# Optimization experiments

Hardware: AMD Instinct MI355X
Metric: run time of the kernel (lower is better)

## Reference

```python
import jax, jax.numpy as jnp
import numpy as np

K_SIZE = 5
SIGMA_IMG = 0.2
SIGMA_VGG = 0.02
BN_EPS = 1e-5
NORM = 2.0  # 2 * len(GPU_IDS), assuming 1 device


def _window_shifts(x, k):
    # x: (n, C, H, W) -> (n, C, H, W, k*k) neighbor values for every offset in
    # the k x k window, zero-padded at image borders.
    r = k // 2
    n, C, H, W = x.shape
    xp = jnp.pad(x, ((0, 0), (0, 0), (r, r), (r, r)))
    cols = [xp[:, :, di:di + H, dj:dj + W] for di in range(k) for dj in range(k)]
    return jnp.stack(cols, axis=-1)


def _modularity(img, seg, k, sigma):
    # img: (n, C, H, W) feature map; seg: (n, K, H, W) soft assignments.
    n, K, H, W = seg.shape
    seg2 = _window_shifts(seg, k)                                  # (n,K,H,W,kk)
    img2 = _window_shifts(img, k)                                  # (n,C,H,W,kk)
    valid = _window_shifts(jnp.ones((1, 1, H, W), img.dtype), k)[:, 0]  # (1,H,W,kk)
    d2 = ((img[..., None] - img2) ** 2).sum(axis=1)                # (n,H,W,kk)
    w12 = jax.lax.stop_gradient(jnp.exp(-d2 / (2.0 * sigma * sigma)) * valid)
    # numerator: sum over pixels & pairs of p1*p2*w12, per (n, K)
    num = jnp.einsum('nkhw,nkhwp,nhwp->nk', seg, seg2, w12)
    # p1 (sum over pairs of p1/n_pairs) == seg; w1 = sum over pairs of w12
    w1 = w12.sum(axis=-1)                                          # (n,H,W)
    den = jnp.einsum('nhw,nkhw->nk', w1, seg)
    rel = num / den                                                # (n,K)
    return rel.sum(axis=1) / (K * n)                               # (n,)


def _conv(x, w, b):
    y = jax.lax.conv_general_dilated(x, w, (1, 1), 'SAME',
                                     dimension_numbers=('NCHW', 'OIHW', 'NCHW'))
    return y + b[None, :, None, None]


def _maxpool2(x):
    return jax.lax.reduce_window(x, -jnp.inf, jax.lax.max,
                                 (1, 1, 2, 2), (1, 1, 2, 2), 'VALID')


def _avgpool2(x):
    n, c, h, w = x.shape
    return x.reshape(n, c, h // 2, 2, w // 2, 2).mean(axis=(3, 5))


def _vgg8(x, w1, b1, w2, b2, w3, b3, w4, b4):
    # VGG16 features[:8]: conv1_1, conv1_2, maxpool, conv2_1, conv2_2 (relu each)
    x = jax.nn.relu(_conv(x, w1, b1))
    x = jax.nn.relu(_conv(x, w2, b2))
    x = _maxpool2(x)
    x = jax.nn.relu(_conv(x, w3, b3))
    x = jax.nn.relu(_conv(x, w4, b4))
    return x


def _batchnorm(x):
    # fresh BatchNorm2d in training mode (weight=1, bias=0), then detach
    m = x.mean(axis=(0, 2, 3), keepdims=True)
    v = x.var(axis=(0, 2, 3), keepdims=True)
    return jax.lax.stop_gradient((x - m) / jnp.sqrt(v + BN_EPS))


def setup_inputs() -> dict:
    key = jax.random.key(0)
    ks = jax.random.split(key, 6)
    images = jax.random.uniform(ks[0], (4, 3, 128, 128), jnp.float32)
    seg = jax.random.uniform(ks[1], (4, 8, 128, 128), jnp.float32)
    segmentation = seg / seg.sum(axis=1, keepdims=True)
    w1 = jax.random.normal(ks[2], (64, 3, 3, 3), jnp.float32) * 0.1
    w2 = jax.random.normal(ks[3], (64, 64, 3, 3), jnp.float32) * 0.05
    w3 = jax.random.normal(ks[4], (128, 64, 3, 3), jnp.float32) * 0.05
    w4 = jax.random.normal(ks[5], (128, 128, 3, 3), jnp.float32) * 0.03
    return {'images': images, 'segmentation': segmentation,
            'w1': w1, 'b1': jnp.zeros(64), 'w2': w2, 'b2': jnp.zeros(64),
            'w3': w3, 'b3': jnp.zeros(128), 'w4': w4, 'b4': jnp.zeros(128)}


def reference(images, segmentation, w1, b1, w2, b2, w3, b3, w4, b4):
    fich = _batchnorm(_vgg8(images, w1, b1, w2, b2, w3, b3, w4, b4))  # (n,128,64,64)
    images_n = _batchnorm(images)
    down_seg = segmentation
    while down_seg.shape[-1] != fich.shape[-1]:
        down_seg = _avgpool2(down_seg)
    loss = (_modularity(fich, down_seg, K_SIZE, SIGMA_VGG).sum()
            + _modularity(images_n, segmentation, K_SIZE, SIGMA_IMG).sum())
    return loss / NORM
```

## Files before the change

### kernel.cpp

```cpp
#include <hip/hip_runtime.h>
#include <hip/hip_bf16.h>
#include <math.h>

typedef __attribute__((ext_vector_type(8))) short short8;
typedef __attribute__((ext_vector_type(4))) float floatx4;
typedef unsigned short ushortT;

__device__ inline short f2bf(float v) {
    __hip_bfloat16 h = __float2bfloat16(v);
    union { __hip_bfloat16 h; short s; } u; u.h = h; return u.s;
}

#define OFF_C2    0
#define OFF_PAD4  8388608
#define OFF_FICH  12849152
#define OFF_PAD2  21237760
#define OFF_PAD3  29890560
#define OFF_WP2   32120832
#define OFF_WP3   32194560
#define OFF_WP4   32342016
#define OFF_ST    33947648
#define OFF_P64   33951744
#define OFF_P128  33968128
#define OFF_PBN   34033664
#define OFF_PIMG  34295808

__global__ __launch_bounds__(256) void prologue(
    char* ws, const float* __restrict__ images,
    const float* __restrict__ w1, const float* __restrict__ b1,
    const float* __restrict__ w2, const float* __restrict__ w3,
    const float* __restrict__ w4)
{
    __shared__ float plds[3 * 720];
    __shared__ float rs[256], rs2[256];

    int b = blockIdx.x;
    int tid = threadIdx.x;

    if (b >= 1362) {
        int bid = b - 1362;
        int txt = bid & 7; bid >>= 3;
        int tyt = bid & 7; bid >>= 3;
        int ocg = bid & 7; bid >>= 3;
        int n = bid;
        int x0 = txt * 16, y0 = tyt * 16;
        int tx = tid & 15, ty = tid >> 4;
        short* outp = (short*)(ws + OFF_PAD2);

        for (int i = tid; i < 972; i += 256) {
            int cc = i / 324; int rem = i - cc * 324;
            int r = rem / 18, c = rem - r * 18;
            int y = y0 - 1 + r, x = x0 - 1 + c;
            float v = 0.f;
            if ((unsigned)y < 128u && (unsigned)x < 128u)
                v = images[((size_t)(n * 3 + cc) * 128 + y) * 128 + x];
            plds[cc * 720 + r * 40 + c] = v;
        }
        __syncthreads();

        float acc[8];
#pragma unroll
        for (int oc = 0; oc < 8; ++oc) acc[oc] = 0.f;
        const float* w_g = w1 + (size_t)(ocg * 8) * 27;
#pragma unroll
        for (int cc = 0; cc < 3; ++cc) {
            const float* base = &plds[cc * 720 + ty * 40 + tx];
            float i00 = base[0],  i01 = base[1],  i02 = base[2];
            float i10 = base[40], i11 = base[41], i12 = base[42];
            float i20 = base[80], i21 = base[81], i22 = base[82];
            const float* wp = w_g + cc * 9;
#pragma unroll
            for (int oc = 0; oc < 8; ++oc) {
                const float* wq = wp + oc * 27;
                float a = acc[oc];
                a = fmaf(wq[0], i00, a); a = fmaf(wq[1], i01, a); a = fmaf(wq[2], i02, a);
                a = fmaf(wq[3], i10, a); a = fmaf(wq[4], i11, a); a = fmaf(wq[5], i12, a);
                a = fmaf(wq[6], i20, a); a = fmaf(wq[7], i21, a); a = fmaf(wq[8], i22, a);
                acc[oc] = a;
            }
        }
        int oy = y0 + ty, ox = x0 + tx;
        short* o = outp + ((size_t)(n * 130 + oy + 1) * 130 + ox + 1) * 64 + ocg * 8;
#pragma unroll
        for (int oc = 0; oc < 8; ++oc) {
            float v = fmaxf(acc[oc] + b1[ocg * 8 + oc], 0.f);
            o[oc] = f2bf(v);
        }
        return;
    }

    if (b < 162) {
        int t = b * 256 + tid;
        short* base; int Hp, Wp, C; int idx;
        if (t < 16512)      { base = (short*)(ws + OFF_PAD2); Hp = 130; Wp = 130; C = 64;  idx = t; }
        else if (t < 24832) { base = (short*)(ws + OFF_PAD3); Hp = 66;  Wp = 66;  C = 64;  idx = t - 16512; }
        else if (t < 41472) { base = (short*)(ws + OFF_PAD4); Hp = 66;  Wp = 66;  C = 128; idx = t - 24832; }
        else return;
        int c8 = idx % (C / 8); int rest = idx / (C / 8);
        int haloPx = 2 * Wp + 2 * (Hp - 2);
        int p = rest % haloPx; int n = rest / haloPx;
        int y, x;
        if (p < Wp)          { y = 0;      x = p; }
        else if (p < 2 * Wp) { y = Hp - 1; x = p - Wp; }
        else { int j = p - 2 * Wp; y = 1 + (j >> 1); x = (j & 1) ? (Wp - 1) : 0; }
        short8 z = {0, 0, 0, 0, 0, 0, 0, 0};
        *(short8*)&base[((size_t)((n * Hp + y) * Wp) + x) * C + c8 * 8] = z;
        return;
    }
    if (b < 1170) {
        int e = (b - 162) * 256 + tid;
        const float* w; short* wp; int CIN, NTALL;
        if (e < 36864)       { w = w2; wp = (short*)(ws + OFF_WP2); CIN = 64;  NTALL = 4; }
        else if (e < 110592) { e -= 36864;  w = w3; wp = (short*)(ws + OFF_WP3); CIN = 64;  NTALL = 8; }
        else if (e < 258048) { e -= 110592; w = w4; wp = (short*)(ws + OFF_WP4); CIN = 128; NTALL = 8; }
        else return;
        int j = e & 7; int L = (e >> 3) & 63; int rest = e >> 9;
        int nt = rest % NTALL; int rest2 = rest / NTALL;
        int KT = CIN / 32;
        int kt = rest2 % KT; int t = rest2 / KT;
        int oc = nt * 16 + (L & 15);
        int ci = kt * 32 + (L >> 4) * 8 + j;
        wp[e] = f2bf(w[((size_t)oc * CIN + ci) * 9 + t]);
        return;
    }
    {
        float* part = (float*)(ws + OFF_PIMG);
        int bb = b - 1170;
        int c = bb >> 6, chunk = bb & 63;
        int base = chunk * 1024 + tid;
        float s = 0.f, s2 = 0.f;
#pragma unroll
        for (int k = 0; k < 4; ++k) {
            int i = base + k * 256;
            int n = i >> 14, hw = i & 16383;
            float v = images[(((size_t)(n * 3 + c)) << 14) + hw];
            s += v; s2 = fmaf(v, v, s2);
        }
        rs[tid] = s; rs2[tid] = s2;
        __syncthreads();
        for (int k = 128; k > 0; k >>= 1) {
            if (tid < k) { rs[tid] += rs[tid + k]; rs2[tid] += rs2[tid + k]; }
            __syncthreads();
        }
        if (tid == 0) { part[bb * 2] = rs[0]; part[bb * 2 + 1] = rs2[0]; }
    }
}

__global__ __launch_bounds__(256) void conv2_pool(
    const short* __restrict__ inp,
    const short* __restrict__ wp,
    const float* __restrict__ bias,
    short* __restrict__ outp)
{
    constexpr int CIN = 64;
    constexpr int Hp = 130, Wp = 130;

    int bid = blockIdx.x;
    int xtb = bid & 1; bid >>= 1;
    int yp = bid & 63; bid >>= 6;
    int n = bid;
    int y0 = yp * 2;
    int x0 = xtb * 64;

    int tid = threadIdx.x;
    int wv = tid >> 6, lane = tid & 63;
    int lm = lane & 15, q = lane >> 4;
    int px0 = x0 + 16 * wv;

    floatx4 acc0[4], acc1[4];
#pragma unroll
    for (int t = 0; t < 4; ++t) {
        acc0[t] = (floatx4){0.f, 0.f, 0.f, 0.f};
        acc1[t] = (floatx4){0.f, 0.f, 0.f, 0.f};
    }

    const short* a_m = inp + lm * CIN + q * 8;
    const short* wbase = wp + (size_t)lane * 8;

    for (int kt = 0; kt < 2; ++kt) {
        int kofs = kt * 32;
#pragma unroll
        for (int s = 0; s < 3; ++s) {
            const short* acol = a_m + ((size_t)((n * Hp + y0) * Wp) + px0 + s) * CIN + kofs;
            short8 av0 = *(const short8*)(acol);
            short8 av1 = *(const short8*)(acol + (size_t)Wp * CIN);
            short8 av2 = *(const short8*)(acol + (size_t)2 * Wp * CIN);
            short8 av3 = *(const short8*)(acol + (size_t)3 * Wp * CIN);
#pragma unroll
            for (int r = 0; r < 3; ++r) {
                const short* bp = wbase + (size_t)(((r * 3 + s) * 2 + kt) * 4) * 512;
                short8 b0 = *(const short8*)bp;
                short8 b1 = *(const short8*)(bp + 512);
                short8 b2 = *(const short8*)(bp + 1024);
                short8 b3 = *(const short8*)(bp + 1536);
                short8 ar  = (r == 0) ? av0 : ((r == 1) ? av1 : av2);
                short8 ar1 = (r == 0) ? av1 : ((r == 1) ? av2 : av3);
                acc0[0] = __builtin_amdgcn_mfma_f32_16x16x32_bf16(ar, b0, acc0[0], 0, 0, 0);
                acc0[1] = __builtin_amdgcn_mfma_f32_16x16x32_bf16(ar, b1, acc0[1], 0, 0, 0);
                acc0[2] = __builtin_amdgcn_mfma_f32_16x16x32_bf16(ar, b2, acc0[2], 0, 0, 0);
                acc0[3] = __builtin_amdgcn_mfma_f32_16x16x32_bf16(ar, b3, acc0[3], 0, 0, 0);
                acc1[0] = __builtin_amdgcn_mfma_f32_16x16x32_bf16(ar1, b0, acc1[0], 0, 0, 0);
                acc1[1] = __builtin_amdgcn_mfma_f32_16x16x32_bf16(ar1, b1, acc1[1], 0, 0, 0);
                acc1[2] = __builtin_amdgcn_mfma_f32_16x16x32_bf16(ar1, b2, acc1[2], 0, 0, 0);
                acc1[3] = __builtin_amdgcn_mfma_f32_16x16x32_bf16(ar1, b3, acc1[3], 0, 0, 0);
            }
        }
    }

    int ox = (px0 + q * 4) >> 1;
#pragma unroll
    for (int t = 0; t < 4; ++t) {
        int oc = t * 16 + lm;
        float bs = bias[oc];
        float v00 = fmaxf(acc0[t][0] + bs, 0.f);
        float v01 = fmaxf(acc0[t][1] + bs, 0.f);
        float v02 = fmaxf(acc0[t][2] + bs, 0.f);
        float v03 = fmaxf(acc0[t][3] + bs, 0.f);
        float v10 = fmaxf(acc1[t][0] + bs, 0.f);
        float v11 = fmaxf(acc1[t][1] + bs, 0.f);
        float v12 = fmaxf(acc1[t][2] + bs, 0.f);
        float v13 = fmaxf(acc1[t][3] + bs, 0.f);
        float m0 = fmaxf(fmaxf(v00, v01), fmaxf(v10, v11));
        float m1 = fmaxf(fmaxf(v02, v03), fmaxf(v12, v13));
        short* o = outp + ((size_t)(n * 66 + yp + 1) * 66 + ox + 1) * 64 + oc;
        o[0]  = f2bf(m0);
        o[64] = f2bf(m1);
    }
}

template<int CIN, int COUT, int H, int W, int OUTMODE>
__global__ __launch_bounds__(256) void conv_mfma2(
    const short* __restrict__ inp, const short* __restrict__ wp,
    const float* __restrict__ bias, void* __restrict__ outv)
{
    constexpr int KT = CIN / 32;
    constexpr int NTALL = COUT / 16;
    constexpr int NTB = COUT / 64;
    constexpr int TPR = W / 64;
    constexpr int Hp = H + 2, Wp = W + 2;

    int bm = blockIdx.x / NTB;
    int bn = blockIdx.x - bm * NTB;
    int n = bm / (H * TPR);
    int rem = bm - n * (H * TPR);
    int y = rem / TPR;
    int x0 = (rem - y * TPR) * 64;

    int tid = threadIdx.x;
    int wv = tid >> 6, lane = tid & 63;
    int lm = lane & 15, q = lane >> 4;
    int px0 = x0 + 16 * wv;
    int ntb = bn * 4;

    floatx4 acc[4];
#pragma unroll
    for (int t = 0; t < 4; ++t) acc[t] = (floatx4){0.f, 0.f, 0.f, 0.f};

    const short* a_m = inp + lm * CIN + q * 8;
    const short* wbase = wp + ((size_t)ntb * 64 + lane) * 8;

    for (int kt = 0; kt < KT; ++kt) {
        int kofs = kt * 32;
#pragma unroll
        for (int r = 0; r < 3; ++r) {
            const short* arow = a_m + (size_t)((n * Hp + y + r) * Wp + px0) * CIN + kofs;
#pragma unroll
            for (int s = 0; s < 3; ++s) {
                short8 av = *(const short8*)(arow + s * CIN);
                const short* bp = wbase + (size_t)(((r * 3 + s) * KT + kt) * NTALL) * 512;
                short8 b0 = *(const short8*)bp;
                short8 b1 = *(const short8*)(bp + 512);
                short8 b2 = *(const short8*)(bp + 1024);
                short8 b3 = *(const short8*)(bp + 1536);
                acc[0] = __builtin_amdgcn_mfma_f32_16x16x32_bf16(av, b0, acc[0], 0, 0, 0);
                acc[1] = __builtin_amdgcn_mfma_f32_16x16x32_bf16(av, b1, acc[1], 0, 0, 0);
                acc[2] = __builtin_amdgcn_mfma_f32_16x16x32_bf16(av, b2, acc[2], 0, 0, 0);
                acc[3] = __builtin_amdgcn_mfma_f32_16x16x32_bf16(av, b3, acc[3], 0, 0, 0);
            }
        }
    }

#pragma unroll
    for (int t = 0; t < 4; ++t) {
        int oc = (ntb + t) * 16 + lm;
        float bs = bias[oc];
#pragma unroll
        for (int i = 0; i < 4; ++i) {
            int px = px0 + q * 4 + i;
            float v = fmaxf(acc[t][i] + bs, 0.f);
            if constexpr (OUTMODE == 0) {
                ((short*)outv)[((size_t)(n * H + y) * W + px) * COUT + oc] = f2bf(v);
            } else if constexpr (OUTMODE == 1) {
                ((short*)outv)[((size_t)(n * Hp + y + 1) * Wp + px + 1) * COUT + oc] = f2bf(v);
            } else {
                ((float*)outv)[((size_t)(n * H + y) * W + px) * COUT + oc] = v;
            }
        }
    }
}

__global__ __launch_bounds__(256) void conv4_bn(
    const short* __restrict__ inp,
    const short* __restrict__ wp,
    const float* __restrict__ bias,
    float* __restrict__ out,
    float* __restrict__ part)
{
    constexpr int CIN = 128;
    constexpr int Hp = 66, Wp = 66;

    int bm = blockIdx.x >> 1;
    int bn = blockIdx.x & 1;
    int n = bm >> 6;
    int y = bm & 63;

    int tid = threadIdx.x;
    int wv = tid >> 6, lane = tid & 63;
    int lm = lane & 15, q = lane >> 4;
    int px0 = 16 * wv;
    int ntb = bn * 4;

    floatx4 acc[4];
#pragma unroll
    for (int t = 0; t < 4; ++t) acc[t] = (floatx4){0.f, 0.f, 0.f, 0.f};

    const short* a_m = inp + lm * CIN + q * 8;
    const short* wbase = wp + ((size_t)ntb * 64 + lane) * 8;

    for (int kt = 0; kt < 4; ++kt) {
        int kofs = kt * 32;
#pragma unroll
        for (int r = 0; r < 3; ++r) {
            const short* arow = a_m + (size_t)((n * Hp + y + r) * Wp + px0) * CIN + kofs;
#pragma unroll
            for (int s = 0; s < 3; ++s) {
                short8 av = *(const short8*)(arow + s * CIN);
                const short* bp = wbase + (size_t)(((r * 3 + s) * 4 + kt) * 8) * 512;
                short8 b0 = *(const short8*)bp;
                short8 b1 = *(const short8*)(bp + 512);
                short8 b2 = *(const short8*)(bp + 1024);
                short8 b3 = *(const short8*)(bp + 1536);
                acc[0] = __builtin_amdgcn_mfma_f32_16x16x32_bf16(av, b0, acc[0], 0, 0, 0);
                acc[1] = __builtin_amdgcn_mfma_f32_16x16x32_bf16(av, b1, acc[1], 0, 0, 0);
                acc[2] = __builtin_amdgcn_mfma_f32_16x16x32_bf16(av, b2, acc[2], 0, 0, 0);
                acc[3] = __builtin_amdgcn_mfma_f32_16x16x32_bf16(av, b3, acc[3], 0, 0, 0);
            }
        }
    }

    __shared__ float ps[4][4][16], ps2[4][4][16];
#pragma unroll
    for (int t = 0; t < 4; ++t) {
        int oc = (ntb + t) * 16 + lm;
        float bs = bias[oc];
        float sv = 0.f, sv2 = 0.f;
#pragma unroll
        for (int i = 0; i < 4; ++i) {
            int px = px0 + q * 4 + i;
            float v = fmaxf(acc[t][i] + bs, 0.f);
            out[((size_t)(n * 64 + y) * 64 + px) * 128 + oc] = v;
            sv += v; sv2 = fmaf(v, v, sv2);
        }
        sv  += __shfl_xor(sv, 16, 64);  sv  += __shfl_xor(sv, 32, 64);
        sv2 += __shfl_xor(sv2, 16, 64); sv2 += __shfl_xor(sv2, 32, 64);
        if (q == 0) { ps[wv][t][lm] = sv; ps2[wv][t][lm] = sv2; }
    }
    __syncthreads();
    if (tid < 64) {
        int t_ = tid >> 4, lm_ = tid & 15;
        float a  = ps[0][t_][lm_] + ps[1][t_][lm_] + ps[2][t_][lm_] + ps[3][t_][lm_];
        float a2 = ps2[0][t_][lm_] + ps2[1][t_][lm_] + ps2[2][t_][lm_] + ps2[3][t_][lm_];
        part[(size_t)blockIdx.x * 128 + tid * 2]     = a;
        part[(size_t)blockIdx.x * 128 + tid * 2 + 1] = a2;
    }
}

__global__ __launch_bounds__(256) void stats_fin(const float* __restrict__ part,
                                                 float* __restrict__ st)
{
    int c = blockIdx.x;
    int t = threadIdx.x;
    int bn = c >> 6, cl = c & 63;
    float s  = part[(size_t)(t * 2 + bn) * 128 + cl * 2];
    float s2 = part[(size_t)(t * 2 + bn) * 128 + cl * 2 + 1];
    __shared__ float rs[256], rs2[256];
    rs[t] = s; rs2[t] = s2;
    __syncthreads();
    for (int k = 128; k > 0; k >>= 1) {
        if (t < k) { rs[t] += rs[t + k]; rs2[t] += rs2[t + k]; }
        __syncthreads();
    }
    if (t == 0) {
        float mean = rs[0] * (1.f / 16384.f);
        float var = rs2[0] * (1.f / 16384.f) - mean * mean;
        st[c] = 1.f / sqrtf(var + 1e-5f);
    }
}

__device__ __forceinline__ void mod64_body(
    int obid,
    const float* __restrict__ xt, const float* __restrict__ seg,
    const float* __restrict__ st, float* __restrict__ part,
    float* fl, float (*sl)[12][14])
{
    int tid = threadIdx.x;
    int w = tid >> 6, lane = tid & 63;
    int tx = lane & 7, ty = lane >> 3;
    int bid = obid;
    int bx = bid & 7; bid >>= 3;
    int by = bid & 7; bid >>= 3;
    int n = bid;
    int x0 = bx * 8, y0 = by * 8;

    for (int i = tid; i < 8 * 144; i += 256) {
        int k = i / 144;
        int rem = i - k * 144;
        int r = rem / 12, c = rem - r * 12;
        int y = y0 - 2 + r, x = x0 - 2 + c;
        float v = 0.f;
        if ((unsigned)y < 64u && (unsigned)x < 64u) {
            const float* p = seg + ((size_t)(n * 8 + k) * 128 + 2 * y) * 128 + 2 * x;
            float2 a = *(const float2*)p;
            float2 b = *(const float2*)(p + 128);
            v = 0.25f * ((a.x + a.y) + (b.x + b.y));
        }
        sl[k][r][c] = v;
    }

    float* slab = fl + w * 2880;

    float d2p[25];
#pragma unroll
    for (int di = 0; di < 5; ++di)
#pragma unroll
        for (int dj = 0; dj < 5; ++dj) {
            int y2 = y0 + ty + di - 2, x2 = x0 + tx + dj - 2;
            float bias = ((unsigned)y2 < 64u && (unsigned)x2 < 64u) ? 0.f : 1e30f;
            d2p[di * 5 + dj] = (w == 0) ? bias : 0.f;
        }

    for (int r8 = 0; r8 < 2; ++r8) {
        int ch0 = w * 32 + r8 * 16;
        for (int i = lane; i < 576; i += 64) {
            int pix = i >> 2, q = i & 3;
            int r = pix / 12, c = pix - r * 12;
            int y = y0 - 2 + r, x = x0 - 2 + c;
            float4 v = make_float4(0.f, 0.f, 0.f, 0.f);
            if ((unsigned)y < 64u && (unsigned)x < 64u) {
                v = *(const float4*)&xt[((size_t)((n * 64 + y) * 64 + x)) * 128 + ch0 + q * 4];
                float4 sv = *(const float4*)&st[ch0 + q * 4];
                v.x *= sv.x; v.y *= sv.y; v.z *= sv.z; v.w *= sv.w;
            }
            *(float4*)&slab[(r * 12 + c) * 20 + q * 4] = v;
        }

        const float* ctr = &slab[((ty + 2) * 12 + tx + 2) * 20];
        float4 c0 = *(const float4*)(ctr + 0);
        float4 c1 = *(const float4*)(ctr + 4);
        float4 c2 = *(const float4*)(ctr + 8);
        float4 c3 = *(const float4*)(ctr + 12);
#pragma unroll
        for (int di = 0; di < 5; ++di)
#pragma unroll
            for (int dj = 0; dj < 5; ++dj) {
                const float* np = &slab[((ty + di) * 12 + tx + dj) * 20];
                float4 v0 = *(const float4*)(np + 0);
                float4 v1 = *(const float4*)(np + 4);
                float4 v2 = *(const float4*)(np + 8);
                float4 v3 = *(const float4*)(np + 12);
                float d = d2p[di * 5 + dj];
                float e;
                e = c0.x - v0.x; d = fmaf(e, e, d);
                e = c0.y - v0.y; d = fmaf(e, e, d);
                e = c0.z - v0.z; d = fmaf(e, e, d);
                e = c0.w - v0.w; d = fmaf(e, e, d);
                e = c1.x - v1.x; d = fmaf(e, e, d);
                e = c1.y - v1.y; d = fmaf(e, e, d);
                e = c1.z - v1.z; d = fmaf(e, e, d);
                e = c1.w - v1.w; d = fmaf(e, e, d);
                e = c2.x - v2.x; d = fmaf(e, e, d);
                e = c2.y - v2.y; d = fmaf(e, e, d);
                e = c2.z - v2.z; d = fmaf(e, e, d);
                e = c2.w - v2.w; d = fmaf(e, e, d);
                e = c3.x - v3.x; d = fmaf(e, e, d);
                e = c3.y - v3.y; d = fmaf(e, e, d);
                e = c3.z - v3.z; d = fmaf(e, e, d);
                e = c3.w - v3.w; d = fmaf(e, e, d);
                d2p[di * 5 + dj] = d;
            }
    }

#pragma unroll
    for (int j = 0; j < 25; ++j) slab[lane * 25 + j] = d2p[j];
    __syncthreads();

    const float minus_inv2s2 = -1.0f / (2.0f * 0.02f * 0.02f);
    for (int i = tid; i < 1600; i += 256) {
        float d = fl[i] + fl[2880 + i] + fl[5760 + i] + fl[8640 + i];
        fl[i] = expf(d * minus_inv2s2);
    }
    __syncthreads();

    float wgt[25];
    float w1 = 0.f;
#pragma unroll
    for (int j = 0; j < 25; ++j) { wgt[j] = fl[lane * 25 + j]; w1 += wgt[j]; }
#pragma unroll
    for (int kk = 0; kk < 2; ++kk) {
        int k = w * 2 + kk;
        float s = 0.f;
#pragma unroll
        for (int di = 0; di < 5; ++di)
#pragma unroll
            for (int dj = 0; dj < 5; ++dj)
                s = fmaf(wgt[di * 5 + dj], sl[k][ty + di][tx + dj], s);
        float sc = sl[k][ty + 2][tx + 2];
        float numk = s * sc;
        float denk = w1 * sc;
#pragma unroll
        for (int sh = 32; sh > 0; sh >>= 1) {
            numk += __shfl_xor(numk, sh, 64);
            denk += __shfl_xor(denk, sh, 64);
        }
        if (lane == 0) {
            part[(size_t)obid * 16 + k * 2] = numk;
            part[(size_t)obid * 16 + k * 2 + 1] = denk;
        }
    }
}

__device__ __forceinline__ void mod128_body(
    int obid,
    const float* __restrict__ img, const float* __restrict__ pimg,
    const float* __restrict__ seg, float* __restrict__ part,
    float (*il)[12][4], float (*sl)[12][14], float* stm)
{
    int t = threadIdx.x;
    int w = t >> 6, lane = t & 63;
    int tx = lane & 7, ty = lane >> 3;

    if (t < 64) {
#pragma unroll
        for (int ch = 0; ch < 3; ++ch) {
            float s  = pimg[(ch * 64 + t) * 2];
            float s2 = pimg[(ch * 64 + t) * 2 + 1];
#pragma unroll
            for (int sh = 32; sh > 0; sh >>= 1) {
                s += __shfl_xor(s, sh, 64);
                s2 += __shfl_xor(s2, sh, 64);
            }
            if (t == 0) {
                float mean = s * (1.f / 65536.f);
                float var = s2 * (1.f / 65536.f) - mean * mean;
                stm[ch] = mean;
                stm[3 + ch] = 1.f / sqrtf(var + 1e-5f);
            }
        }
    }

    int bid = obid;
    int bx = bid & 15; bid >>= 4;
    int by = bid & 15; bid >>= 4;
    int n = bid;
    int x0 = bx * 8, y0 = by * 8;

    for (int i = t; i < 8 * 144; i += 256) {
        int k = i / 144;
        int rem = i - k * 144;
        int r = rem / 12, c = rem - r * 12;
        int y = y0 - 2 + r, x = x0 - 2 + c;
        float v = 0.f;
        if ((unsigned)y < 128u && (unsigned)x < 128u)
            v = seg[((size_t)(n * 8 + k) * 128 + y) * 128 + x];
        sl[k][r][c] = v;
    }
    __syncthreads();

    float mn0 = stm[0], mn1 = stm[1], mn2 = stm[2];
    float rs0 = stm[3], rs1 = stm[4], rs2 = stm[5];

    for (int i = t; i < 432; i += 256) {
        int ch = i / 144; int pix = i - ch * 144;
        int r = pix / 12, c = pix - r * 12;
        int y = y0 - 2 + r, x = x0 - 2 + c;
        float v = 0.f;
        if ((unsigned)y < 128u && (unsigned)x < 128u) {
            float raw = img[(((size_t)(n * 3 + ch)) << 14) + y * 128 + x];
            float mn = ch == 0 ? mn0 : (ch == 1 ? mn1 : mn2);
            float rs = ch == 0 ? rs0 : (ch == 1 ? rs1 : rs2);
            v = (raw - mn) * rs;
        }
        il[r][c][ch] = v;
    }
    __syncthreads();

    const float minus_inv2s2 = -1.0f / (2.0f * 0.2f * 0.2f);
    float c0 = il[ty + 2][tx + 2][0];
    float c1 = il[ty + 2][tx + 2][1];
    float c2 = il[ty + 2][tx + 2][2];

    float wgt[25];
    float w1 = 0.f;
#pragma unroll
    for (int di = 0; di < 5; ++di)
#pragma unroll
        for (int dj = 0; dj < 5; ++dj) {
            int y2 = y0 + ty + di - 2, x2 = x0 + tx + dj - 2;
            float bias = ((unsigned)y2 < 128u && (unsigned)x2 < 128u) ? 0.f : 1e30f;
            const float* np = &il[ty + di][tx + dj][0];
            float e0 = c0 - np[0], e1 = c1 - np[1], e2 = c2 - np[2];
            float d = bias + fmaf(e2, e2, fmaf(e1, e1, e0 * e0));
            float wv = expf(d * minus_inv2s2);
            wgt[di * 5 + dj] = wv;
            w1 += wv;
        }

#pragma unroll
    for (int kk = 0; kk < 2; ++kk) {
        int k = w * 2 + kk;
        float s = 0.f;
#pragma unroll
        for (int di = 0; di < 5; ++di)
#pragma unroll
            for (int dj = 0; dj < 5; ++dj)
                s = fmaf(wgt[di * 5 + dj], sl[k][ty + di][tx + dj], s);
        float sc = sl[k][ty + 2][tx + 2];
        float numk = s * sc;
        float denk = w1 * sc;
#pragma unroll
        for (int sft = 32; sft > 0; sft >>= 1) {
            numk += __shfl_xor(numk, sft, 64);
            denk += __shfl_xor(denk, sft, 64);
        }
        if (lane == 0) {
            part[(size_t)obid * 16 + k * 2] = numk;
            part[(size_t)obid * 16 + k * 2 + 1] = denk;
        }
    }
}

__global__ __launch_bounds__(256) void modularity_all(
    const float* __restrict__ xt,
    const float* __restrict__ seg,
    const float* __restrict__ st,
    const float* __restrict__ img,
    const float* __restrict__ pimg,
    float* __restrict__ p64, float* __restrict__ p128)
{
    __shared__ float fl[4 * 2880];
    __shared__ float sl[8][12][14];
    __shared__ float stm[6];

    int bid = blockIdx.x;
    int g = bid / 5;
    int r5 = bid - g * 5;
    if (r5 == 0) {
        mod64_body(g, xt, seg, st, p64, fl, sl);
    } else {
        mod128_body(bid - g - 1, img, pimg, seg, p128,
                    (float(*)[12][4])fl, sl, stm);
    }
}

__global__ __launch_bounds__(1024) void reduce_finalize(
    const float* __restrict__ p64, const float* __restrict__ p128,
    float* __restrict__ out)
{
    int t = threadIdx.x;
    int j = t >> 4, s = t & 15;
    float num = 0.f, den = 0.f;
    if (j < 32) {
        int n = j >> 3, k = j & 7;
#pragma unroll
        for (int i = 0; i < 4; ++i) {
            int b = s * 4 + i;
            const float* p = p64 + ((size_t)(n * 64 + b)) * 16 + k * 2;
            num += p[0]; den += p[1];
        }
    } else {
        int jj = j - 32; int n = jj >> 3, k = jj & 7;
#pragma unroll
        for (int i = 0; i < 16; ++i) {
            int b = s * 16 + i;
            const float* p = p128 + ((size_t)(n * 256 + b)) * 16 + k * 2;
            num += p[0]; den += p[1];
        }
    }
#pragma unroll
    for (int sh = 8; sh > 0; sh >>= 1) {
        num += __shfl_xor(num, sh, 16);
        den += __shfl_xor(den, sh, 16);
    }
    __shared__ float rn[64], rd[64];
    if (s == 0) { rn[j] = num; rd[j] = den; }
    __syncthreads();
    if (t < 64) {
        float v = rn[t] / rd[t];
#pragma unroll
        for (int sh = 32; sh > 0; sh >>= 1) v += __shfl_xor(v, sh, 64);
        if (t == 0) out[0] = v * (1.0f / 64.0f);
    }
}

extern "C" void kernel_launch(void* const* d_in, const int* in_sizes, int n_in,
                              void* d_out, int out_size, void* d_ws, size_t ws_size,
                              hipStream_t stream)
{
    const float* images = (const float*)d_in[0];
    const float* seg    = (const float*)d_in[1];
    const float* w1 = (const float*)d_in[2]; const float* b1 = (const float*)d_in[3];
    const float* w2 = (const float*)d_in[4]; const float* b2 = (const float*)d_in[5];
    const float* w3 = (const float*)d_in[6]; const float* b3 = (const float*)d_in[7];
    const float* w4 = (const float*)d_in[8]; const float* b4 = (const float*)d_in[9];
    float* out = (float*)d_out;
    char* ws = (char*)d_ws;
    short* PAD2 = (short*)(ws + OFF_PAD2);
    short* PAD3 = (short*)(ws + OFF_PAD3);
    short* PAD4 = (short*)(ws + OFF_PAD4);
    float* FICH = (float*)(ws + OFF_FICH);
    short* WP2  = (short*)(ws + OFF_WP2);
    short* WP3  = (short*)(ws + OFF_WP3);
    short* WP4  = (short*)(ws + OFF_WP4);
    float* ST   = (float*)(ws + OFF_ST);
    float* P64  = (float*)(ws + OFF_P64);
    float* P128 = (float*)(ws + OFF_P128);
    float* PBN  = (float*)(ws + OFF_PBN);
    float* PIMG = (float*)(ws + OFF_PIMG);

    prologue<<<3410, 256, 0, stream>>>(ws, images, w1, b1, w2, w3, w4);
    conv2_pool<<<512, 256, 0, stream>>>(PAD2, WP2, b2, PAD3);
    conv_mfma2<64, 128, 64, 64, 1><<<512, 256, 0, stream>>>(PAD3, WP3, b3, PAD4);
    conv4_bn<<<512, 256, 0, stream>>>(PAD4, WP4, b4, FICH, PBN);
    stats_fin<<<128, 256, 0, stream>>>(PBN, ST);
    modularity_all<<<1280, 256, 0, stream>>>(FICH, seg, ST, images, PIMG, P64, P128);
    reduce_finalize<<<1, 1024, 0, stream>>>(P64, P128, out);
}
```

Measured before the change: 166.7 us.

## Retile conv kernels for row reuse and fold BN stats and final reduce into modularity

Conv2 and conv3/conv4 now compute several output rows per block and load each input row once for reuse across the 3 kernel rows, while each block covers fewer output channels. The batchnorm statistics finalize kernel is removed: every mod64 block recomputes the per-channel inverse std from the partial sums. The final reduction kernel is replaced by a last-block-done atomic counter inside modularity_all. expf becomes __expf. Together these cut two launches and redundant activation loads, at the cost of redundant stats work per block and a less precise exp.

Result: slower. 192.3 us (+15.4%).

```diff
diff --git a/kernel.cpp b/kernel.cpp
--- a/kernel.cpp
+++ b/kernel.cpp
@@ -9,6 +9,12 @@
 __device__ inline short f2bf(float v) {
     __hip_bfloat16 h = __float2bfloat16(v);
     union { __hip_bfloat16 h; short s; } u; u.h = h; return u.s;
+}
+__device__ inline void gstore(float* p, float v) {
+    __hip_atomic_store(p, v, __ATOMIC_RELAXED, __HIP_MEMORY_SCOPE_AGENT);
+}
+__device__ inline float gload(const float* p) {
+    return __hip_atomic_load(p, __ATOMIC_RELAXED, __HIP_MEMORY_SCOPE_AGENT);
 }
 
 #define OFF_C2    0
@@ -19,7 +25,7 @@
 #define OFF_WP2   32120832
 #define OFF_WP3   32194560
 #define OFF_WP4   32342016
-#define OFF_ST    33947648
+#define OFF_CNT   33947648
 #define OFF_P64   33951744
 #define OFF_P128  33968128
 #define OFF_PBN   34033664
@@ -36,6 +42,8 @@
 
     int b = blockIdx.x;
     int tid = threadIdx.x;
+
+    if (b == 0 && tid == 0) *(int*)(ws + OFF_CNT) = 0;
 
     if (b >= 1362) {
         int bid = b - 1362;
@@ -156,105 +164,101 @@
     constexpr int Hp = 130, Wp = 130;
 
     int bid = blockIdx.x;
-    int xtb = bid & 1; bid >>= 1;
-    int yp = bid & 63; bid >>= 6;
+    int o2 = bid & 1; bid >>= 1;
+    int xt = bid & 1; bid >>= 1;
+    int yq = bid & 31; bid >>= 5;
     int n = bid;
-    int y0 = yp * 2;
-    int x0 = xtb * 64;
+    int y0 = yq * 4;
+    int x0 = xt * 64;
 
     int tid = threadIdx.x;
     int wv = tid >> 6, lane = tid & 63;
     int lm = lane & 15, q = lane >> 4;
     int px0 = x0 + 16 * wv;
-
-    floatx4 acc0[4], acc1[4];
-#pragma unroll
-    for (int t = 0; t < 4; ++t) {
-        acc0[t] = (floatx4){0.f, 0.f, 0.f, 0.f};
-        acc1[t] = (floatx4){0.f, 0.f, 0.f, 0.f};
-    }
+    int ntb = o2 * 2;
+
+    floatx4 acc[4][2];
+#pragma unroll
+    for (int d = 0; d < 4; ++d)
+#pragma unroll
+        for (int t = 0; t < 2; ++t) acc[d][t] = (floatx4){0.f, 0.f, 0.f, 0.f};
 
     const short* a_m = inp + lm * CIN + q * 8;
-    const short* wbase = wp + (size_t)lane * 8;
+    const short* wbase = wp + ((size_t)ntb * 64 + lane) * 8;
 
     for (int kt = 0; kt < 2; ++kt) {
         int kofs = kt * 32;
 #pragma unroll
         for (int s = 0; s < 3; ++s) {
             const short* acol = a_m + ((size_t)((n * Hp + y0) * Wp) + px0 + s) * CIN + kofs;
-            short8 av0 = *(const short8*)(acol);
-            short8 av1 = *(const short8*)(acol + (size_t)Wp * CIN);
-            short8 av2 = *(const short8*)(acol + (size_t)2 * Wp * CIN);
-            short8 av3 = *(const short8*)(acol + (size_t)3 * Wp * CIN);
+            short8 av[6];
+#pragma unroll
+            for (int j = 0; j < 6; ++j)
+                av[j] = *(const short8*)(acol + (size_t)j * Wp * CIN);
 #pragma unroll
             for (int r = 0; r < 3; ++r) {
                 const short* bp = wbase + (size_t)(((r * 3 + s) * 2 + kt) * 4) * 512;
                 short8 b0 = *(const short8*)bp;
                 short8 b1 = *(const short8*)(bp + 512);
-                short8 b2 = *(const short8*)(bp + 1024);
-                short8 b3 = *(const short8*)(bp + 1536);
-                short8 ar  = (r == 0) ? av0 : ((r == 1) ? av1 : av2);
-                short8 ar1 = (r == 0) ? av1 : ((r == 1) ? av2 : av3);
-                acc0[0] = __builtin_amdgcn_mfma_f32_16x16x32_bf16(ar, b0, acc0[0], 0, 0, 0);
-                acc0[1] = __builtin_amdgcn_mfma_f32_16x16x32_bf16(ar, b1, acc0[1], 0, 0, 0);
-                acc0[2] = __builtin_amdgcn_mfma_f32_16x16x32_bf16(ar, b2, acc0[2], 0, 0, 0);
-                acc0[3] = __builtin_amdgcn_mfma_f32_16x16x32_bf16(ar, b3, acc0[3], 0, 0, 0);
-                acc1[0] = __builtin_amdgcn_mfma_f32_16x16x32_bf16(ar1, b0, acc1[0], 0, 0, 0);
-                acc1[1] = __builtin_amdgcn_mfma_f32_16x16x32_bf16(ar1, b1, acc1[1], 0, 0, 0);
-                acc1[2] = __builtin_amdgcn_mfma_f32_16x16x32_bf16(ar1, b2, acc1[2], 0, 0, 0);
-                acc1[3] = __builtin_amdgcn_mfma_f32_16x16x32_bf16(ar1, b3, acc1[3], 0, 0, 0);
+#pragma unroll
+                for (int d = 0; d < 4; ++d) {
+                    acc[d][0] = __builtin_amdgcn_mfma_f32_16x16x32_bf16(av[r + d], b0, acc[d][0], 0, 0, 0);
+                    acc[d][1] = __builtin_amdgcn_mfma_f32_16x16x32_bf16(av[r + d], b1, acc[d][1], 0, 0, 0);
+                }
             }
         }
     }
 
     int ox = (px0 + q * 4) >> 1;
 #pragma unroll
-    for (int t = 0; t < 4; ++t) {
-        int oc = t * 16 + lm;
+    for (int t2 = 0; t2 < 2; ++t2) {
+        int oc = (ntb + t2) * 16 + lm;
         float bs = bias[oc];
-        float v00 = fmaxf(acc0[t][0] + bs, 0.f);
-        float v01 = fmaxf(acc0[t][1] + bs, 0.f);
-        float v02 = fmaxf(acc0[t][2] + bs, 0.f);
-        float v03 = fmaxf(acc0[t][3] + bs, 0.f);
-        float v10 = fmaxf(acc1[t][0] + bs, 0.f);
-        float v11 = fmaxf(acc1[t][1] + bs, 0.f);
-        float v12 = fmaxf(acc1[t][2] + bs, 0.f);
-        float v13 = fmaxf(acc1[t][3] + bs, 0.f);
-        float m0 = fmaxf(fmaxf(v00, v01), fmaxf(v10, v11));
-        float m1 = fmaxf(fmaxf(v02, v03), fmaxf(v12, v13));
-        short* o = outp + ((size_t)(n * 66 + yp + 1) * 66 + ox + 1) * 64 + oc;
-        o[0]  = f2bf(m0);
-        o[64] = f2bf(m1);
-    }
-}
-
-template<int CIN, int COUT, int H, int W, int OUTMODE>
-__global__ __launch_bounds__(256) void conv_mfma2(
-    const short* __restrict__ inp, const short* __restrict__ wp,
-    const float* __restrict__ bias, void* __restrict__ outv)
+#pragma unroll
+        for (int p = 0; p < 2; ++p) {
+            float v00 = fmaxf(acc[2 * p][t2][0] + bs, 0.f);
+            float v01 = fmaxf(acc[2 * p][t2][1] + bs, 0.f);
+            float v02 = fmaxf(acc[2 * p][t2][2] + bs, 0.f);
+            float v03 = fmaxf(acc[2 * p][t2][3] + bs, 0.f);
+            float v10 = fmaxf(acc[2 * p + 1][t2][0] + bs, 0.f);
+            float v11 = fmaxf(acc[2 * p + 1][t2][1] + bs, 0.f);
+            float v12 = fmaxf(acc[2 * p + 1][t2][2] + bs, 0.f);
+            float v13 = fmaxf(acc[2 * p + 1][t2][3] + bs, 0.f);
+            float m0 = fmaxf(fmaxf(v00, v01), fmaxf(v10, v11));
+            float m1 = fmaxf(fmaxf(v02, v03), fmaxf(v12, v13));
+            int oy = yq * 2 + p;
+            short* o = outp + ((size_t)(n * 66 + oy + 1) * 66 + ox + 1) * 64 + oc;
+            o[0]  = f2bf(m0);
+            o[64] = f2bf(m1);
+        }
+    }
+}
+
+__global__ __launch_bounds__(256) void conv3_2row(
+    const short* __restrict__ inp,
+    const short* __restrict__ wp,
+    const float* __restrict__ bias,
+    short* __restrict__ outp)
 {
-    constexpr int KT = CIN / 32;
-    constexpr int NTALL = COUT / 16;
-    constexpr int NTB = COUT / 64;
-    constexpr int TPR = W / 64;
-    constexpr int Hp = H + 2, Wp = W + 2;
-
-    int bm = blockIdx.x / NTB;
-    int bn = blockIdx.x - bm * NTB;
-    int n = bm / (H * TPR);
-    int rem = bm - n * (H * TPR);
-    int y = rem / TPR;
-    int x0 = (rem - y * TPR) * 64;
+    constexpr int CIN = 64, COUT = 128, Hp = 66, Wp = 66, KT = 2, NTALL = 8;
+
+    int bid = blockIdx.x;
+    int bn = bid & 3; bid >>= 2;
+    int yq = bid & 31; bid >>= 5;
+    int n = bid;
+    int y0 = yq * 2;
 
     int tid = threadIdx.x;
     int wv = tid >> 6, lane = tid & 63;
     int lm = lane & 15, q = lane >> 4;
-    int px0 = x0 + 16 * wv;
-    int ntb = bn * 4;
-
-    floatx4 acc[4];
-#pragma unroll
-    for (int t = 0; t < 4; ++t) acc[t] = (floatx4){0.f, 0.f, 0.f, 0.f};
+    int px0 = 16 * wv;
+    int ntb = bn * 2;
+
+    floatx4 acc[2][2];
+#pragma unroll
+    for (int d = 0; d < 2; ++d)
+#pragma unroll
+        for (int t = 0; t < 2; ++t) acc[d][t] = (floatx4){0.f, 0.f, 0.f, 0.f};
 
     const short* a_m = inp + lm * CIN + q * 8;
     const short* wbase = wp + ((size_t)ntb * 64 + lane) * 8;
@@ -262,38 +266,37 @@
     for (int kt = 0; kt < KT; ++kt) {
         int kofs = kt * 32;
 #pragma unroll
-        for (int r = 0; r < 3; ++r) {
-            const short* arow = a_m + (size_t)((n * Hp + y + r) * Wp + px0) * CIN + kofs;
-#pragma unroll
-            for (int s = 0; s < 3; ++s) {
-                short8 av = *(const short8*)(arow + s * CIN);
+        for (int s = 0; s < 3; ++s) {
+            const short* acol = a_m + ((size_t)((n * Hp + y0) * Wp) + px0 + s) * CIN + kofs;
+            short8 av[4];
+#pragma unroll
+            for (int j = 0; j < 4; ++j)
+                av[j] = *(const short8*)(acol + (size_t)j * Wp * CIN);
+#pragma unroll
+            for (int r = 0; r < 3; ++r) {
                 const short* bp = wbase + (size_t)(((r * 3 + s) * KT + kt) * NTALL) * 512;
                 short8 b0 = *(const short8*)bp;
                 short8 b1 = *(const short8*)(bp + 512);
-                short8 b2 = *(const short8*)(bp + 1024);
-                short8 b3 = *(const short8*)(bp + 1536);
-                acc[0] = __builtin_amdgcn_mfma_f32_16x16x32_bf16(av, b0, acc[0], 0, 0, 0);
-                acc[1] = __builtin_amdgcn_mfma_f32_16x16x32_bf16(av, b1, acc[1], 0, 0, 0);
-                acc[2] = __builtin_amdgcn_mfma_f32_16x16x32_bf16(av, b2, acc[2], 0, 0, 0);
-                acc[3] = __builtin_amdgcn_mfma_f32_16x16x32_bf16(av, b3, acc[3], 0, 0, 0);
-            }
-        }
-    }
-
-#pragma unroll
-    for (int t = 0; t < 4; ++t) {
-        int oc = (ntb + t) * 16 + lm;
+#pragma unroll
+                for (int d = 0; d < 2; ++d) {
+                    acc[d][0] = __builtin_amdgcn_mfma_f32_16x16x32_bf16(av[r + d], b0, acc[d][0], 0, 0, 0);
+                    acc[d][1] = __builtin_amdgcn_mfma_f32_16x16x32_bf16(av[r + d], b1, acc[d][1], 0, 0, 0);
+                }
+            }
+        }
+    }
+
+#pragma unroll
+    for (int t2 = 0; t2 < 2; ++t2) {
+        int oc = (ntb + t2) * 16 + lm;
         float bs = bias[oc];
 #pragma unroll
-        for (int i = 0; i < 4; ++i) {
-            int px = px0 + q * 4 + i;
-            float v = fmaxf(acc[t][i] + bs, 0.f);
-            if constexpr (OUTMODE == 0) {
-                ((short*)outv)[((size_t)(n * H + y) * W + px) * COUT + oc] = f2bf(v);
-            } else if constexpr (OUTMODE == 1) {
-                ((short*)outv)[((size_t)(n * Hp + y + 1) * Wp + px + 1) * COUT + oc] = f2bf(v);
-            } else {
-                ((float*)outv)[((size_t)(n * H + y) * W + px) * COUT + oc] = v;
+        for (int d = 0; d < 2; ++d) {
+#pragma unroll
+            for (int i = 0; i < 4; ++i) {
+                int px = px0 + q * 4 + i;
+                float v = fmaxf(acc[d][t2][i] + bs, 0.f);
+                outp[((size_t)(n * Hp + y0 + d + 1) * Wp + px + 1) * COUT + oc] = f2bf(v);
             }
         }
     }
@@ -306,102 +309,87 @@
     float* __restrict__ out,
     float* __restrict__ part)
 {
-    constexpr int CIN = 128;
-    constexpr int Hp = 66, Wp = 66;
-
-    int bm = blockIdx.x >> 1;
-    int bn = blockIdx.x & 1;
-    int n = bm >> 6;
-    int y = bm & 63;
+    constexpr int CIN = 128, Hp = 66, Wp = 66, KT = 4, NTALL = 8;
+
+    int bid = blockIdx.x;
+    int bn = bid & 3; bid >>= 2;
+    int yq = bid & 31; bid >>= 5;
+    int n = bid;
+    int y0 = yq * 2;
 
     int tid = threadIdx.x;
     int wv = tid >> 6, lane = tid & 63;
     int lm = lane & 15, q = lane >> 4;
     int px0 = 16 * wv;
-    int ntb = bn * 4;
-
-    floatx4 acc[4];
-#pragma unroll
-    for (int t = 0; t < 4; ++t) acc[t] = (floatx4){0.f, 0.f, 0.f, 0.f};
+    int ntb = bn * 2;
+
+    floatx4 acc[2][2];
+#pragma unroll
+    for (int d = 0; d < 2; ++d)
+#pragma unroll
+        for (int t = 0; t < 2; ++t) acc[d][t] = (floatx4){0.f, 0.f, 0.f, 0.f};
 
     const short* a_m = inp + lm * CIN + q * 8;
     const short* wbase = wp + ((size_t)ntb * 64 + lane) * 8;
 
-    for (int kt = 0; kt < 4; ++kt) {
+    for (int kt = 0; kt < KT; ++kt) {
         int kofs = kt * 32;
 #pragma unroll
-        for (int r = 0; r < 3; ++r) {
-            const short* arow = a_m + (size_t)((n * Hp + y + r) * Wp + px0) * CIN + kofs;
-#pragma unroll
-            for (int s = 0; s < 3; ++s) {
-                short8 av = *(const short8*)(arow + s * CIN);
-                const short* bp = wbase + (size_t)(((r * 3 + s) * 4 + kt) * 8) * 512;
+        for (int s = 0; s < 3; ++s) {
+            const short* acol = a_m + ((size_t)((n * Hp + y0) * Wp) + px0 + s) * CIN + kofs;
+            short8 av[4];
+#pragma unroll
+            for (int j = 0; j < 4; ++j)
+                av[j] = *(const short8*)(acol + (size_t)j * Wp * CIN);
+#pragma unroll
+            for (int r = 0; r < 3; ++r) {
+                const short* bp = wbase + (size_t)(((r * 3 + s) * KT + kt) * NTALL) * 512;
                 short8 b0 = *(const short8*)bp;
                 short8 b1 = *(const short8*)(bp + 512);
-                short8 b2 = *(const short8*)(bp + 1024);
-                short8 b3 = *(const short8*)(bp + 1536);
-                acc[0] = __builtin_amdgcn_mfma_f32_16x16x32_bf16(av, b0, acc[0], 0, 0, 0);
-                acc[1] = __builtin_amdgcn_mfma_f32_16x16x32_bf16(av, b1, acc[1], 0, 0, 0);
-                acc[2] = __builtin_amdgcn_mfma_f32_16x16x32_bf16(av, b2, acc[2], 0, 0, 0);
-                acc[3] = __builtin_amdgcn_mfma_f32_16x16x32_bf16(av, b3, acc[3], 0, 0, 0);
-            }
-        }
-    }
-
-    __shared__ float ps[4][4][16], ps2[4][4][16];
-#pragma unroll
-    for (int t = 0; t < 4; ++t) {
-        int oc = (ntb + t) * 16 + lm;
+#pragma unroll
+                for (int d = 0; d < 2; ++d) {
+                    acc[d][0] = __builtin_amdgcn_mfma_f32_16x16x32_bf16(av[r + d], b0, acc[d][0], 0, 0, 0);
+                    acc[d][1] = __builtin_amdgcn_mfma_f32_16x16x32_bf16(av[r + d], b1, acc[d][1], 0, 0, 0);
+                }
+            }
+        }
+    }
+
+    __shared__ float ps[4][2][16], ps2[4][2][16];
+#pragma unroll
+    for (int t2 = 0; t2 < 2; ++t2) {
+        int oc = (ntb + t2) * 16 + lm;
         float bs = bias[oc];
         float sv = 0.f, sv2 = 0.f;
 #pragma unroll
-        for (int i = 0; i < 4; ++i) {
-            int px = px0 + q * 4 + i;
-            float v = fmaxf(acc[t][i] + bs, 0.f);
-            out[((size_t)(n * 64 + y) * 64 + px) * 128 + oc] = v;
-            sv += v; sv2 = fmaf(v, v, sv2);
+        for (int d = 0; d < 2; ++d) {
+#pragma unroll
+            for (int i = 0; i < 4; ++i) {
+                int px = px0 + q * 4 + i;
+                float v = fmaxf(acc[d][t2][i] + bs, 0.f);
+                out[((size_t)(n * 64 + y0 + d) * 64 + px) * 128 + oc] = v;
+                sv += v; sv2 = fmaf(v, v, sv2);
+            }
         }
         sv  += __shfl_xor(sv, 16, 64);  sv  += __shfl_xor(sv, 32, 64);
         sv2 += __shfl_xor(sv2, 16, 64); sv2 += __shfl_xor(sv2, 32, 64);
-        if (q == 0) { ps[wv][t][lm] = sv; ps2[wv][t][lm] = sv2; }
+        if (q == 0) { ps[wv][t2][lm] = sv; ps2[wv][t2][lm] = sv2; }
     }
     __syncthreads();
-    if (tid < 64) {
+    if (tid < 32) {
         int t_ = tid >> 4, lm_ = tid & 15;
         float a  = ps[0][t_][lm_] + ps[1][t_][lm_] + ps[2][t_][lm_] + ps[3][t_][lm_];
         float a2 = ps2[0][t_][lm_] + ps2[1][t_][lm_] + ps2[2][t_][lm_] + ps2[3][t_][lm_];
-        part[(size_t)blockIdx.x * 128 + tid * 2]     = a;
-        part[(size_t)blockIdx.x * 128 + tid * 2 + 1] = a2;
-    }
-}
-
-__global__ __launch_bounds__(256) void stats_fin(const float* __restrict__ part,
-                                                 float* __restrict__ st)
-{
-    int c = blockIdx.x;
-    int t = threadIdx.x;
-    int bn = c >> 6, cl = c & 63;
-    float s  = part[(size_t)(t * 2 + bn) * 128 + cl * 2];
-    float s2 = part[(size_t)(t * 2 + bn) * 128 + cl * 2 + 1];
-    __shared__ float rs[256], rs2[256];
-    rs[t] = s; rs2[t] = s2;
-    __syncthreads();
-    for (int k = 128; k > 0; k >>= 1) {
-        if (t < k) { rs[t] += rs[t + k]; rs2[t] += rs2[t + k]; }
-        __syncthreads();
-    }
-    if (t == 0) {
-        float mean = rs[0] * (1.f / 16384.f);
-        float var = rs2[0] * (1.f / 16384.f) - mean * mean;
-        st[c] = 1.f / sqrtf(var + 1e-5f);
+        part[(size_t)blockIdx.x * 64 + tid * 2]     = a;
+        part[(size_t)blockIdx.x * 64 + tid * 2 + 1] = a2;
     }
 }
 
 __device__ __forceinline__ void mod64_body(
     int obid,
     const float* __restrict__ xt, const float* __restrict__ seg,
-    const float* __restrict__ st, float* __restrict__ part,
-    float* fl, float (*sl)[12][14])
+    const float* __restrict__ pbn, float* __restrict__ part,
+    float* fl, float (*sl)[12][14], float* stf)
 {
     int tid = threadIdx.x;
     int w = tid >> 6, lane = tid & 63;
@@ -427,6 +415,28 @@
         sl[k][r][c] = v;
     }
 
+    {
+        int c = tid & 127, h = tid >> 7;
+        int bnq = c >> 5, lc = c & 31;
+        float s = 0.f, s2 = 0.f;
+        const float* pb = pbn + lc * 2;
+        for (int i = 0; i < 64; ++i) {
+            int b = (h * 64 + i) * 4 + bnq;
+            float2 v = *(const float2*)(pb + (size_t)b * 64);
+            s += v.x; s2 += v.y;
+        }
+        fl[tid] = s; fl[256 + tid] = s2;
+        __syncthreads();
+        if (tid < 128) {
+            float ss = fl[tid] + fl[tid + 128];
+            float qq = fl[256 + tid] + fl[256 + tid + 128];
+            float mean = ss * (1.f / 16384.f);
+            float var = qq * (1.f / 16384.f) - mean * mean;
+            stf[tid] = 1.f / sqrtf(var + 1e-5f);
+        }
+        __syncthreads();
+    }
+
     float* slab = fl + w * 2880;
 
     float d2p[25];
@@ -448,7 +458,7 @@
             float4 v = make_float4(0.f, 0.f, 0.f, 0.f);
             if ((unsigned)y < 64u && (unsigned)x < 64u) {
                 v = *(const float4*)&xt[((size_t)((n * 64 + y) * 64 + x)) * 128 + ch0 + q * 4];
-                float4 sv = *(const float4*)&st[ch0 + q * 4];
+                float4 sv = *(const float4*)&stf[ch0 + q * 4];
                 v.x *= sv.x; v.y *= sv.y; v.z *= sv.z; v.w *= sv.w;
             }
             *(float4*)&slab[(r * 12 + c) * 20 + q * 4] = v;
@@ -523,8 +533,8 @@
             denk += __shfl_xor(denk, sh, 64);
         }
         if (lane == 0) {
-            part[(size_t)obid * 16 + k * 2] = numk;
-            part[(size_t)obid * 16 + k * 2 + 1] = denk;
+            gstore(&part[(size_t)obid * 16 + k * 2], numk);
+            gstore(&part[(size_t)obid * 16 + k * 2 + 1], denk);
         }
     }
 }
@@ -610,7 +620,7 @@
             const float* np = &il[ty + di][tx + dj][0];
             float e0 = c0 - np[0], e1 = c1 - np[1], e2 = c2 - np[2];
             float d = bias + fmaf(e2, e2, fmaf(e1, e1, e0 * e0));
-            float wv = expf(d * minus_inv2s2);
+            float wv = __expf(d * minus_inv2s2);
             wgt[di * 5 + dj] = wv;
             w1 += wv;
         }
@@ -633,8 +643,8 @@
             denk += __shfl_xor(denk, sft, 64);
         }
         if (lane == 0) {
-            part[(size_t)obid * 16 + k * 2] = numk;
-            part[(size_t)obid * 16 + k * 2 + 1] = denk;
+            gstore(&part[(size_t)obid * 16 + k * 2], numk);
+            gstore(&part[(size_t)obid * 16 + k * 2 + 1], denk);
         }
     }
 }
@@ -642,63 +652,63 @@
 __global__ __launch_bounds__(256) void modularity_all(
     const float* __restrict__ xt,
     const float* __restrict__ seg,
-    const float* __restrict__ st,
+    const float* __restrict__ pbn,
     const float* __restrict__ img,
     const float* __restrict__ pimg,
-    float* __restrict__ p64, float* __restrict__ p128)
+    float* __restrict__ p64, float* __restrict__ p128,
+    float* __restrict__ out, int* __restrict__ cnt)
 {
     __shared__ float fl[4 * 2880];
     __shared__ float sl[8][12][14];
     __shared__ float stm[6];
+    __shared__ __align__(16) float stf[128];
+    __shared__ int lastf;
 
     int bid = blockIdx.x;
+    int tid = threadIdx.x;
     int g = bid / 5;
     int r5 = bid - g * 5;
     if (r5 == 0) {
-        mod64_body(g, xt, seg, st, p64, fl, sl);
+        mod64_body(g, xt, seg, pbn, p64, fl, sl, stf);
     } else {
         mod128_body(bid - g - 1, img, pimg, seg, p128,
                     (float(*)[12][4])fl, sl, stm);
     }
-}
-
-__global__ __launch_bounds__(1024) void reduce_finalize(
-    const float* __restrict__ p64, const float* __restrict__ p128,
-    float* __restrict__ out)
-{
-    int t = threadIdx.x;
-    int j = t >> 4, s = t & 15;
+
+    __syncthreads();
+    if (tid == 0) {
+        int old = __hip_atomic_fetch_add(cnt, 1, __ATOMIC_ACQ_REL, __HIP_MEMORY_SCOPE_AGENT);
+        lastf = (old == 1279);
+    }
+    __syncthreads();
+    if (!lastf) return;
+
+    int j = tid >> 2, s4 = tid & 3;
     float num = 0.f, den = 0.f;
     if (j < 32) {
         int n = j >> 3, k = j & 7;
-#pragma unroll
-        for (int i = 0; i < 4; ++i) {
-            int b = s * 4 + i;
+        for (int i = 0; i < 16; ++i) {
+            int b = s4 * 16 + i;
             const float* p = p64 + ((size_t)(n * 64 + b)) * 16 + k * 2;
-            num += p[0]; den += p[1];
+            num += gload(p); den += gload(p + 1);
         }
     } else {
         int jj = j - 32; int n = jj >> 3, k = jj & 7;
-#pragma unroll
-        for (int i = 0; i < 16; ++i) {
-            int b = s * 16 + i;
+        for (int i = 0; i < 64; ++i) {
+            int b = s4 * 64 + i;
             const float* p = p128 + ((size_t)(n * 256 + b)) * 16 + k * 2;
-            num += p[0]; den += p[1];
-        }
-    }
-#pragma unroll
-    for (int sh = 8; sh > 0; sh >>= 1) {
-        num += __shfl_xor(num, sh, 16);
-        den += __shfl_xor(den, sh, 16);
-    }
-    __shared__ float rn[64], rd[64];
-    if (s == 0) { rn[j] = num; rd[j] = den; }
+            num += gload(p); den += gload(p + 1);
+        }
+    }
+    num += __shfl_xor(num, 1, 64); den += __shfl_xor(den, 1, 64);
+    num += __shfl_xor(num, 2, 64); den += __shfl_xor(den, 2, 64);
+    if (s4 == 0) { fl[j] = num; fl[64 + j] = den; }
     __syncthreads();
-    if (t < 64) {
-        float v = rn[t] / rd[t];
+    if (tid < 64) {
+        float v = fl[tid] / fl[64 + tid];
 #pragma unroll
         for (int sh = 32; sh > 0; sh >>= 1) v += __shfl_xor(v, sh, 64);
-        if (t == 0) out[0] = v * (1.0f / 64.0f);
+        if (tid == 0) out[0] = v * (1.0f / 64.0f);
     }
 }
 
@@ -721,17 +731,16 @@
     short* WP2  = (short*)(ws + OFF_WP2);
     short* WP3  = (short*)(ws + OFF_WP3);
     short* WP4  = (short*)(ws + OFF_WP4);
-    float* ST   = (float*)(ws + OFF_ST);
     float* P64  = (float*)(ws + OFF_P64);
     float* P128 = (float*)(ws + OFF_P128);
     float* PBN  = (float*)(ws + OFF_PBN);
     float* PIMG = (float*)(ws + OFF_PIMG);
+    int*   CNT  = (int*)(ws + OFF_CNT);
 
     prologue<<<3410, 256, 0, stream>>>(ws, images, w1, b1, w2, w3, w4);
     conv2_pool<<<512, 256, 0, stream>>>(PAD2, WP2, b2, PAD3);
-    conv_mfma2<64, 128, 64, 64, 1><<<512, 256, 0, stream>>>(PAD3, WP3, b3, PAD4);
+    conv3_2row<<<512, 256, 0, stream>>>(PAD3, WP3, b3, PAD4);
     conv4_bn<<<512, 256, 0, stream>>>(PAD4, WP4, b4, FICH, PBN);
-    stats_fin<<<128, 256, 0, stream>>>(PBN, ST);
-    modularity_all<<<1280, 256, 0, stream>>>(FICH, seg, ST, images, PIMG, P64, P128);
-    reduce_finalize<<<1, 1024, 0, stream>>>(P64, P128, out);
-}
+    modularity_all<<<1280, 256, 0, stream>>>(FICH, seg, PBN, images, PIMG,
+                                             P64, P128, out, CNT);
+}
```
